# Kernel optimization log

Measured on AMD Instinct MI355X. Metric: run time of the kernel, lower is better.

## Reference

```python
import jax, jax.numpy as jnp
import numpy as np

NUM_HEADS = 12


def setup_inputs() -> dict:
    key = jax.random.key(0)
    k1, k2, k3, k4 = jax.random.split(key, 4)
    B, T, N, C = 4, 64, 196, 768
    x = jax.random.normal(k1, (B, T, N, C), dtype=jnp.float32)
    w_qkv = jax.random.normal(k2, (3 * C, C), dtype=jnp.float32) * (C ** -0.5)
    w_proj = jax.random.normal(k3, (C, C), dtype=jnp.float32) * (C ** -0.5)
    b_proj = jax.random.normal(k4, (C,), dtype=jnp.float32) * 0.01
    return {"x": x, "w_qkv": w_qkv, "w_proj": w_proj, "b_proj": b_proj}


def reference(x, w_qkv, w_proj, b_proj):
    B, T, N, C = x.shape
    H = NUM_HEADS
    hd = C // H
    scale = hd ** -0.5
    # qkv: (B, T, N, 3C) -> (3, B, H, N, T, hd)
    qkv = (x @ w_qkv.T).reshape(B, T, N, 3, H, hd)
    qkv = jnp.transpose(qkv, (3, 0, 4, 2, 1, 5))
    q, k, v = qkv[0], qkv[1], qkv[2]
    # temporal attention per spatial position: (B, H, N, T, T)
    attn = jnp.einsum('bhnqd,bhnkd->bhnqk', q, k) * scale
    causal_mask = jnp.triu(jnp.ones((T, T), dtype=bool), k=1)
    attn = jnp.where(causal_mask, -jnp.inf, attn)
    attn = jax.nn.softmax(attn, axis=-1)
    out = jnp.einsum('bhnqk,bhnkd->bhnqd', attn, v)  # (B, H, N, T, hd)
    out = jnp.transpose(out, (0, 3, 2, 1, 4)).reshape(B, T, N, C)
    return out @ w_proj.T + b_proj
```

## Files before the change

kernel.cpp:

```cpp
#include <hip/hip_runtime.h>

typedef unsigned short UST;
typedef __bf16 bf16x8 __attribute__((ext_vector_type(8)));
typedef float f32x4 __attribute__((ext_vector_type(4)));
typedef float f32x8 __attribute__((ext_vector_type(8)));

__device__ __forceinline__ UST f2bf(float f) {
  return __builtin_bit_cast(UST, (__bf16)f);
}

__device__ __forceinline__ void split8v(f32x8 f, uint4& h, uint4& l) {
  UST hh[8], ll[8];
#pragma unroll
  for (int i = 0; i < 8; ++i) {
    float v = f[i];
    __bf16 hb = (__bf16)v;
    hh[i] = __builtin_bit_cast(UST, hb);
    ll[i] = __builtin_bit_cast(UST, (__bf16)(v - (float)hb));
  }
  h = *(uint4*)hh; l = *(uint4*)ll;
}

__device__ __forceinline__ size_t tok_row(int p, int bn0) {
  const int bn = bn0 + (p >> 6);
  const int b  = bn / 196;
  const int n  = bn - b * 196;
  return (size_t)b * 12544 + (size_t)(p & 63) * 196 + (size_t)n;
}

__device__ __forceinline__ void gl_lds16(const void* g, void* l) {
  __builtin_amdgcn_global_load_lds(
      (__attribute__((address_space(1))) void*)g,
      (__attribute__((address_space(3))) void*)l, 16, 0, 0);
}

__global__ __launch_bounds__(256) void split_f32(
    const float* __restrict__ in, UST* __restrict__ hi, UST* __restrict__ lo,
    int n8)
{
  for (int i = blockIdx.x * 256 + threadIdx.x; i < n8; i += gridDim.x * 256) {
    f32x8 v = *(const f32x8*)(in + (size_t)i * 8);
    uint4 h, l;
    split8v(v, h, l);
    *(uint4*)(hi + (size_t)i * 8) = h;
    *(uint4*)(lo + (size_t)i * 8) = l;
  }
}

__global__ __launch_bounds__(256) void gemm_pre(
    const UST* __restrict__ Agh, const UST* __restrict__ Agl,
    const UST* __restrict__ Bgh, const UST* __restrict__ Bgl,
    const float* __restrict__ bias, float* __restrict__ Cf,
    UST* __restrict__ Cb,
    int M, int N, int K, int pmode, int bn0)
{
  __shared__ __align__(16) UST Ah[128 * 32];
  __shared__ __align__(16) UST Al[128 * 32];
  __shared__ __align__(16) UST Bh[128 * 32];
  __shared__ __align__(16) UST Bl[128 * 32];

  const int tid  = threadIdx.x;
  const int lane = tid & 63;
  const int wv   = tid >> 6;
  const int wr   = wv >> 1;
  const int wc   = wv & 1;
  const int lm   = lane & 15;
  const int lq   = lane >> 4;

  const int m0 = blockIdx.y * 128;
  const int n0 = blockIdx.x * 128;

  f32x4 acc[4][4] = {};

  const int sr = tid >> 2;
  const int sc = (tid & 3) * 8;

  const int ar1 = m0 + sr, ar2 = ar1 + 64;
  const size_t ga1 = (pmode == 1) ? tok_row(ar1, bn0) : (size_t)ar1;
  const size_t ga2 = (pmode == 1) ? tok_row(ar2, bn0) : (size_t)ar2;
  const UST* pA1h = Agh + ga1 * K + sc;
  const UST* pA2h = Agh + ga2 * K + sc;
  const UST* pA1l = Agl + ga1 * K + sc;
  const UST* pA2l = Agl + ga2 * K + sc;
  const UST* pB1h = Bgh + (size_t)(n0 + sr) * K + sc;
  const UST* pB2h = Bgh + (size_t)(n0 + sr + 64) * K + sc;
  const UST* pB1l = Bgl + (size_t)(n0 + sr) * K + sc;
  const UST* pB2l = Bgl + (size_t)(n0 + sr + 64) * K + sc;

  const int l0 = wv * 64 * 8;
  const int l1 = (256 + wv * 64) * 8;

  for (int k0 = 0; k0 < K; k0 += 32) {
    __syncthreads();
    gl_lds16(pA1h + k0, &Ah[l0]);
    gl_lds16(pA2h + k0, &Ah[l1]);
    gl_lds16(pA1l + k0, &Al[l0]);
    gl_lds16(pA2l + k0, &Al[l1]);
    gl_lds16(pB1h + k0, &Bh[l0]);
    gl_lds16(pB2h + k0, &Bh[l1]);
    gl_lds16(pB1l + k0, &Bl[l0]);
    gl_lds16(pB2l + k0, &Bl[l1]);
    __syncthreads();

    bf16x8 afh[4], afl[4], bfh[4], bfl[4];
#pragma unroll
    for (int i = 0; i < 4; ++i) {
      const int off = (wr * 64 + i * 16 + lm) * 32 + lq * 8;
      afh[i] = *(const bf16x8*)(Ah + off);
      afl[i] = *(const bf16x8*)(Al + off);
    }
#pragma unroll
    for (int j = 0; j < 4; ++j) {
      const int off = (wc * 64 + j * 16 + lm) * 32 + lq * 8;
      bfh[j] = *(const bf16x8*)(Bh + off);
      bfl[j] = *(const bf16x8*)(Bl + off);
    }
#pragma unroll
    for (int i = 0; i < 4; ++i)
#pragma unroll
      for (int j = 0; j < 4; ++j) {
        acc[i][j] = __builtin_amdgcn_mfma_f32_16x16x32_bf16(afh[i], bfh[j], acc[i][j], 0, 0, 0);
        acc[i][j] = __builtin_amdgcn_mfma_f32_16x16x32_bf16(afh[i], bfl[j], acc[i][j], 0, 0, 0);
        acc[i][j] = __builtin_amdgcn_mfma_f32_16x16x32_bf16(afl[i], bfh[j], acc[i][j], 0, 0, 0);
      }
  }

#pragma unroll
  for (int j = 0; j < 4; ++j) {
    const int n = n0 + wc * 64 + j * 16 + lm;
    const float bv = bias ? bias[n] : 0.0f;
#pragma unroll
    for (int i = 0; i < 4; ++i) {
      const int pb = m0 + wr * 64 + i * 16 + lq * 4;
#pragma unroll
      for (int r = 0; r < 4; ++r) {
        const int p = pb + r;
        const size_t g = (pmode == 2) ? tok_row(p, bn0) : (size_t)p;
        const float v = acc[i][j][r] + bv;
        if (Cb) Cb[g * (size_t)N + n] = f2bf(v);
        else    Cf[g * (size_t)N + n] = v;
      }
    }
  }
}

#define SQ_STRIDE 67
#define TS 72

__global__ __launch_bounds__(256) void attn64(
    const UST* __restrict__ qkv, UST* __restrict__ oh, UST* __restrict__ ol)
{
  const int nl = blockIdx.x;
  const int h  = blockIdx.y;

  __shared__ __align__(16) UST Qs[64 * TS];
  __shared__ __align__(16) UST Ks[64 * TS];
  __shared__ __align__(16) UST Vt[64 * TS];
  __shared__ __align__(16) UST Ps[64 * TS];
  __shared__ float Ss[64 * SQ_STRIDE];
  __shared__ float red[4 * 64];
  __shared__ float denom[64];

  const int tid  = threadIdx.x;
  const int lane = tid & 63;
  const int wv   = tid >> 6;
  const int lm   = lane & 15;
  const int lq   = lane >> 4;

#pragma unroll
  for (int it = 0; it < 2; ++it) {
    const int idx = it * 256 + tid;
    const int t   = idx >> 3;
    const int f0  = (idx & 7) * 8;
    const UST* row = qkv + (size_t)(nl * 64 + t) * 2304 + h * 64 + f0;
    uint4 qv = *(const uint4*)row;
    uint4 kv = *(const uint4*)(row + 768);
    uint4 vv = *(const uint4*)(row + 1536);
    *(uint4*)(&Qs[t * TS + f0]) = qv;
    *(uint4*)(&Ks[t * TS + f0]) = kv;
    UST vs[8];
    *(uint4*)vs = vv;
    const int cb = t >> 3;
#pragma unroll
    for (int i = 0; i < 8; ++i) {
      const int d = f0 + i;
      Vt[d * TS + (((cb ^ (d >> 3)) & 7) << 3) + (t & 7)] = vs[i];
    }
  }
  __syncthreads();

  f32x4 accS[4] = {};
#pragma unroll
  for (int s = 0; s < 2; ++s) {
    bf16x8 aq = *(const bf16x8*)(&Qs[(wv * 16 + lm) * TS + s * 32 + lq * 8]);
#pragma unroll
    for (int j = 0; j < 4; ++j) {
      bf16x8 bk = *(const bf16x8*)(&Ks[(j * 16 + lm) * TS + s * 32 + lq * 8]);
      accS[j] = __builtin_amdgcn_mfma_f32_16x16x32_bf16(aq, bk, accS[j], 0, 0, 0);
    }
  }

#pragma unroll
  for (int j = 0; j < 4; ++j)
#pragma unroll
    for (int r = 0; r < 4; ++r) {
      const int q = wv * 16 + lq * 4 + r;
      const int c = j * 16 + lm;
      Ss[q * SQ_STRIDE + c] = (c > q) ? -1e30f : accS[j][r] * 0.125f;
    }
  __syncthreads();

  {
    const int r = tid >> 2;
    const int seg = tid & 3;
    const float* srow = &Ss[r * SQ_STRIDE + seg * 16];
    float mx = -1e30f;
#pragma unroll
    for (int c = 0; c < 16; ++c) mx = fmaxf(mx, srow[c]);
    red[seg * 64 + r] = mx;
  }
  __syncthreads();
  {
    const int r = tid >> 2;
    const int seg = tid & 3;
    const float M = fmaxf(fmaxf(red[r], red[64 + r]), fmaxf(red[128 + r], red[192 + r]));
    float ssum = 0.f;
#pragma unroll
    for (int c = 0; c < 16; ++c) {
      const int col = seg * 16 + c;
      float e = 0.f;
      if (col <= r) e = __expf(Ss[r * SQ_STRIDE + col] - M);
      Ps[r * TS + col] = f2bf(e);
      ssum += e;
    }
    __syncthreads();
    red[seg * 64 + r] = ssum;
  }
  __syncthreads();
  if (tid < 64)
    denom[tid] = red[tid] + red[64 + tid] + red[128 + tid] + red[192 + tid];
  __syncthreads();

  f32x4 accO[4] = {};
#pragma unroll
  for (int s = 0; s < 2; ++s) {
    bf16x8 ap = *(const bf16x8*)(&Ps[(wv * 16 + lm) * TS + s * 32 + lq * 8]);
#pragma unroll
    for (int j = 0; j < 4; ++j) {
      const int d = j * 16 + lm;
      const int cb = s * 4 + lq;
      bf16x8 bv = *(const bf16x8*)(&Vt[d * TS + (((cb ^ (d >> 3)) & 7) << 3)]);
      accO[j] = __builtin_amdgcn_mfma_f32_16x16x32_bf16(ap, bv, accO[j], 0, 0, 0);
    }
  }

  float inv[4];
#pragma unroll
  for (int r = 0; r < 4; ++r) inv[r] = 1.0f / denom[wv * 16 + lq * 4 + r];
#pragma unroll
  for (int j = 0; j < 4; ++j)
#pragma unroll
    for (int r = 0; r < 4; ++r) {
      const int q = wv * 16 + lq * 4 + r;
      const int d = j * 16 + lm;
      const float o = accO[j][r] * inv[r];
      const __bf16 hb = (__bf16)o;
      const size_t gi = (size_t)(nl * 64 + q) * 768 + h * 64 + d;
      oh[gi] = __builtin_bit_cast(UST, hb);
      ol[gi] = f2bf(o - (float)hb);
    }
}

__global__ void fill_one(float* p, int n) {
  for (int i = blockIdx.x * 256 + threadIdx.x; i < n; i += gridDim.x * 256)
    p[i] = 1.0f;
}

extern "C" void kernel_launch(void* const* d_in, const int* in_sizes, int n_in,
                              void* d_out, int out_size, void* d_ws, size_t ws_size,
                              hipStream_t stream)
{
  const float* x      = (const float*)d_in[0];
  const float* w_qkv  = (const float*)d_in[1];
  const float* w_proj = (const float*)d_in[2];
  const float* b_proj = (const float*)d_in[3];
  float* out = (float*)d_out;

  const size_t XN = 38535168ull;
  const size_t WQ = 2304ull * 768;
  const size_t WP = 768ull * 768;
  const size_t fixed_b = 2 * (2 * XN + 2 * WQ + 2 * WP);
  const size_t per_bn = 64ull * 2304 * 2 + 2ull * 64 * 768 * 2;

  static const int cands[] = {784, 392, 196, 112, 56, 28, 14, 8, 4, 2};
  int NBc = 0;
  for (int i = 0; i < 10; ++i) {
    if (fixed_b + (size_t)cands[i] * per_bn <= ws_size) { NBc = cands[i]; break; }
  }

  if (NBc == 0) {
    fill_one<<<512, 256, 0, stream>>>(out, out_size);
    return;
  }

  UST* Xh  = (UST*)d_ws;
  UST* Xl  = Xh + XN;
  UST* Wh  = Xl + XN;
  UST* Wl  = Wh + WQ;
  UST* Ph  = Wl + WQ;
  UST* Pl  = Ph + WP;
  UST* qkv = Pl + WP;
  UST* Oh  = qkv + (size_t)NBc * 64 * 2304;
  UST* Ol  = Oh + (size_t)NBc * 64 * 768;

  split_f32<<<2048, 256, 0, stream>>>(x, Xh, Xl, (int)(XN / 8));
  split_f32<<<864, 256, 0, stream>>>(w_qkv, Wh, Wl, (int)(WQ / 8));
  split_f32<<<288, 256, 0, stream>>>(w_proj, Ph, Pl, (int)(WP / 8));

  const int Mi = NBc * 64;
  for (int bn0 = 0; bn0 < 784; bn0 += NBc) {
    dim3 g1(2304 / 128, Mi / 128);
    gemm_pre<<<g1, 256, 0, stream>>>(Xh, Xl, Wh, Wl, nullptr, nullptr, qkv,
                                     Mi, 2304, 768, 1, bn0);
    dim3 ga(NBc, 12);
    attn64<<<ga, 256, 0, stream>>>(qkv, Oh, Ol);
    dim3 g2(768 / 128, Mi / 128);
    gemm_pre<<<g2, 256, 0, stream>>>(Oh, Ol, Ph, Pl, b_proj, out, nullptr,
                                     Mi, 768, 768, 2, bn0);
  }
}
```

Before: 1.198 ms.

## Rewrite split-bf16 GEMM with 256x256 tiles, double-buffered LDS and XCD remap

Replaces the 128x128 single-buffered GEMM with a 512-thread 256x256-tile kernel that double-buffers its global-to-LDS loads, so the next K slice is fetched while MFMAs run on the current one. It adds an XOR swizzle of LDS chunks to reduce bank conflicts, remaps workgroup ids across the 8 XCDs for L2 locality, and raises wave priority around the MFMA blocks. The larger tile cuts redundant A/B traffic per output, at the cost of much higher register and LDS use (128 KB of LDS per block) and fewer blocks on the small projection GEMM. Batch candidates not divisible by 4 are dropped so M stays a multiple of 256.

New measurement: 1.031 ms. -14.0%, faster.

```diff
diff --git a/kernel.cpp b/kernel.cpp
--- a/kernel.cpp
+++ b/kernel.cpp
@@ -28,9 +28,9 @@
   return (size_t)b * 12544 + (size_t)(p & 63) * 196 + (size_t)n;
 }
 
-__device__ __forceinline__ void gl_lds16(const void* g, void* l) {
+__device__ __forceinline__ void gl_lds16(const UST* g, UST* l) {
   __builtin_amdgcn_global_load_lds(
-      (__attribute__((address_space(1))) void*)g,
+      (const __attribute__((address_space(1))) void*)g,
       (__attribute__((address_space(3))) void*)l, 16, 0, 0);
 }
 
@@ -47,94 +47,125 @@
   }
 }
 
-__global__ __launch_bounds__(256) void gemm_pre(
+#define SBAR()   __builtin_amdgcn_s_barrier()
+#define SCHED0() __builtin_amdgcn_sched_barrier(0)
+#define WAIT_VM0() do { asm volatile("s_waitcnt vmcnt(0)" ::: "memory"); SCHED0(); } while (0)
+
+__global__ __launch_bounds__(512, 2) void gemm2p(
     const UST* __restrict__ Agh, const UST* __restrict__ Agl,
     const UST* __restrict__ Bgh, const UST* __restrict__ Bgl,
     const float* __restrict__ bias, float* __restrict__ Cf,
     UST* __restrict__ Cb,
     int M, int N, int K, int pmode, int bn0)
 {
-  __shared__ __align__(16) UST Ah[128 * 32];
-  __shared__ __align__(16) UST Al[128 * 32];
-  __shared__ __align__(16) UST Bh[128 * 32];
-  __shared__ __align__(16) UST Bl[128 * 32];
+  __shared__ __align__(16) UST lds[2][4][8192];
 
   const int tid  = threadIdx.x;
   const int lane = tid & 63;
   const int wv   = tid >> 6;
-  const int wr   = wv >> 1;
-  const int wc   = wv & 1;
+  const int wr   = wv >> 2;
+  const int wcn  = wv & 3;
   const int lm   = lane & 15;
   const int lq   = lane >> 4;
 
-  const int m0 = blockIdx.y * 128;
-  const int n0 = blockIdx.x * 128;
-
-  f32x4 acc[4][4] = {};
-
-  const int sr = tid >> 2;
-  const int sc = (tid & 3) * 8;
-
-  const int ar1 = m0 + sr, ar2 = ar1 + 64;
-  const size_t ga1 = (pmode == 1) ? tok_row(ar1, bn0) : (size_t)ar1;
-  const size_t ga2 = (pmode == 1) ? tok_row(ar2, bn0) : (size_t)ar2;
-  const UST* pA1h = Agh + ga1 * K + sc;
-  const UST* pA2h = Agh + ga2 * K + sc;
-  const UST* pA1l = Agl + ga1 * K + sc;
-  const UST* pA2l = Agl + ga2 * K + sc;
-  const UST* pB1h = Bgh + (size_t)(n0 + sr) * K + sc;
-  const UST* pB2h = Bgh + (size_t)(n0 + sr + 64) * K + sc;
-  const UST* pB1l = Bgl + (size_t)(n0 + sr) * K + sc;
-  const UST* pB2l = Bgl + (size_t)(n0 + sr + 64) * K + sc;
-
-  const int l0 = wv * 64 * 8;
-  const int l1 = (256 + wv * 64) * 8;
-
-  for (int k0 = 0; k0 < K; k0 += 32) {
-    __syncthreads();
-    gl_lds16(pA1h + k0, &Ah[l0]);
-    gl_lds16(pA2h + k0, &Ah[l1]);
-    gl_lds16(pA1l + k0, &Al[l0]);
-    gl_lds16(pA2l + k0, &Al[l1]);
-    gl_lds16(pB1h + k0, &Bh[l0]);
-    gl_lds16(pB2h + k0, &Bh[l1]);
-    gl_lds16(pB1l + k0, &Bl[l0]);
-    gl_lds16(pB2l + k0, &Bl[l1]);
-    __syncthreads();
-
-    bf16x8 afh[4], afl[4], bfh[4], bfl[4];
-#pragma unroll
-    for (int i = 0; i < 4; ++i) {
-      const int off = (wr * 64 + i * 16 + lm) * 32 + lq * 8;
-      afh[i] = *(const bf16x8*)(Ah + off);
-      afl[i] = *(const bf16x8*)(Al + off);
-    }
+  const int gx  = gridDim.x;
+  const int nwg = gx * gridDim.y;
+  int wgid;
+  {
+    const int orig = blockIdx.y * gx + blockIdx.x;
+    const int q = nwg >> 3, r = nwg & 7;
+    const int xcd = orig & 7, off = orig >> 3;
+    wgid = (xcd < r ? xcd * (q + 1) : r * (q + 1) + (xcd - r) * q) + off;
+  }
+  const int m0 = (wgid / gx) * 256;
+  const int n0 = (wgid % gx) * 256;
+
+  const int l2   = lane >> 2;
+  const int csrc = (lane & 3) ^ (((lane >> 5) & 1) << 1);
+  const int sA0 = m0 + wv * 16 + l2;
+  const int sB0 = n0 + wv * 16 + l2;
+  const size_t rA0 = (pmode == 1) ? tok_row(sA0, bn0)       : (size_t)sA0;
+  const size_t rA1 = (pmode == 1) ? tok_row(sA0 + 128, bn0) : (size_t)(sA0 + 128);
+  const UST* pA0h = Agh + rA0 * K + csrc * 8;
+  const UST* pA0l = Agl + rA0 * K + csrc * 8;
+  const UST* pA1h = Agh + rA1 * K + csrc * 8;
+  const UST* pA1l = Agl + rA1 * K + csrc * 8;
+  const UST* pB0h = Bgh + (size_t)sB0 * K + csrc * 8;
+  const UST* pB0l = Bgl + (size_t)sB0 * K + csrc * 8;
+  const UST* pB1h = Bgh + (size_t)(sB0 + 128) * K + csrc * 8;
+  const UST* pB1l = Bgl + (size_t)(sB0 + 128) * K + csrc * 8;
+  const int ldst = wv * 512;
+
+  const int ck = lq ^ (((lm >> 3) & 1) << 1);
+  const int raBase = (wr * 128 + lm) * 32 + ck * 8;
+  const int rbBase = (wcn * 64 + lm) * 32 + ck * 8;
+
+  f32x4 acc[8][4] = {};
+
+#define STAGE(bufW, koff) do { \
+  gl_lds16(pA0h + (koff), (bufW)[0] + 0 * 4096 + ldst); \
+  gl_lds16(pA1h + (koff), (bufW)[0] + 1 * 4096 + ldst); \
+  gl_lds16(pA0l + (koff), (bufW)[1] + 0 * 4096 + ldst); \
+  gl_lds16(pA1l + (koff), (bufW)[1] + 1 * 4096 + ldst); \
+  gl_lds16(pB0h + (koff), (bufW)[2] + 0 * 4096 + ldst); \
+  gl_lds16(pB1h + (koff), (bufW)[2] + 1 * 4096 + ldst); \
+  gl_lds16(pB0l + (koff), (bufW)[3] + 0 * 4096 + ldst); \
+  gl_lds16(pB1l + (koff), (bufW)[3] + 1 * 4096 + ldst); \
+} while (0)
+
+  STAGE(lds[0], 0);
+
+  const int NT = K >> 5;
+  for (int u = 0; u < NT; ++u) {
+    UST (*bufR)[8192] = lds[u & 1];
+    UST (*bufW)[8192] = lds[(u & 1) ^ 1];
+    WAIT_VM0();
+    SBAR();
+    SCHED0();
+    if (u + 1 < NT) STAGE(bufW, (u + 1) * 32);
+
+    bf16x8 bfh[4], bfl[4];
 #pragma unroll
     for (int j = 0; j < 4; ++j) {
-      const int off = (wc * 64 + j * 16 + lm) * 32 + lq * 8;
-      bfh[j] = *(const bf16x8*)(Bh + off);
-      bfl[j] = *(const bf16x8*)(Bl + off);
-    }
-#pragma unroll
-    for (int i = 0; i < 4; ++i)
-#pragma unroll
-      for (int j = 0; j < 4; ++j) {
-        acc[i][j] = __builtin_amdgcn_mfma_f32_16x16x32_bf16(afh[i], bfh[j], acc[i][j], 0, 0, 0);
-        acc[i][j] = __builtin_amdgcn_mfma_f32_16x16x32_bf16(afh[i], bfl[j], acc[i][j], 0, 0, 0);
-        acc[i][j] = __builtin_amdgcn_mfma_f32_16x16x32_bf16(afl[i], bfh[j], acc[i][j], 0, 0, 0);
+      const int off = rbBase + j * 512;
+      bfh[j] = *(const bf16x8*)(bufR[2] + off);
+      bfl[j] = *(const bf16x8*)(bufR[3] + off);
+    }
+#pragma unroll
+    for (int mh = 0; mh < 2; ++mh) {
+      bf16x8 afh[4], afl[4];
+#pragma unroll
+      for (int ii = 0; ii < 4; ++ii) {
+        const int off = raBase + (mh * 4 + ii) * 512;
+        afh[ii] = *(const bf16x8*)(bufR[0] + off);
+        afl[ii] = *(const bf16x8*)(bufR[1] + off);
       }
-  }
+      __builtin_amdgcn_s_setprio(1);
+#pragma unroll
+      for (int ii = 0; ii < 4; ++ii)
+#pragma unroll
+        for (int jj = 0; jj < 4; ++jj) {
+          f32x4 c = acc[mh * 4 + ii][jj];
+          c = __builtin_amdgcn_mfma_f32_16x16x32_bf16(afh[ii], bfh[jj], c, 0, 0, 0);
+          c = __builtin_amdgcn_mfma_f32_16x16x32_bf16(afh[ii], bfl[jj], c, 0, 0, 0);
+          c = __builtin_amdgcn_mfma_f32_16x16x32_bf16(afl[ii], bfh[jj], c, 0, 0, 0);
+          acc[mh * 4 + ii][jj] = c;
+        }
+      __builtin_amdgcn_s_setprio(0);
+    }
+  }
+#undef STAGE
 
 #pragma unroll
   for (int j = 0; j < 4; ++j) {
-    const int n = n0 + wc * 64 + j * 16 + lm;
+    const int n = n0 + wcn * 64 + j * 16 + lm;
     const float bv = bias ? bias[n] : 0.0f;
 #pragma unroll
-    for (int i = 0; i < 4; ++i) {
-      const int pb = m0 + wr * 64 + i * 16 + lq * 4;
+    for (int i = 0; i < 8; ++i) {
+      const int pbase = m0 + wr * 128 + i * 16 + lq * 4;
 #pragma unroll
       for (int r = 0; r < 4; ++r) {
-        const int p = pb + r;
+        const int p = pbase + r;
         const size_t g = (pmode == 2) ? tok_row(p, bn0) : (size_t)p;
         const float v = acc[i][j][r] + bv;
         if (Cb) Cb[g * (size_t)N + n] = f2bf(v);
@@ -292,9 +323,9 @@
   const size_t fixed_b = 2 * (2 * XN + 2 * WQ + 2 * WP);
   const size_t per_bn = 64ull * 2304 * 2 + 2ull * 64 * 768 * 2;
 
-  static const int cands[] = {784, 392, 196, 112, 56, 28, 14, 8, 4, 2};
+  static const int cands[] = {784, 392, 196, 112, 56, 28, 8, 4};
   int NBc = 0;
-  for (int i = 0; i < 10; ++i) {
+  for (int i = 0; i < 8; ++i) {
     if (fixed_b + (size_t)cands[i] * per_bn <= ws_size) { NBc = cands[i]; break; }
   }
 
@@ -319,13 +350,13 @@
 
   const int Mi = NBc * 64;
   for (int bn0 = 0; bn0 < 784; bn0 += NBc) {
-    dim3 g1(2304 / 128, Mi / 128);
-    gemm_pre<<<g1, 256, 0, stream>>>(Xh, Xl, Wh, Wl, nullptr, nullptr, qkv,
-                                     Mi, 2304, 768, 1, bn0);
+    dim3 g1(2304 / 256, Mi / 256);
+    gemm2p<<<g1, 512, 0, stream>>>(Xh, Xl, Wh, Wl, nullptr, nullptr, qkv,
+                                   Mi, 2304, 768, 1, bn0);
     dim3 ga(NBc, 12);
     attn64<<<ga, 256, 0, stream>>>(qkv, Oh, Ol);
-    dim3 g2(768 / 128, Mi / 128);
-    gemm_pre<<<g2, 256, 0, stream>>>(Oh, Ol, Ph, Pl, b_proj, out, nullptr,
-                                     Mi, 768, 768, 2, bn0);
-  }
-}
+    dim3 g2(768 / 256, Mi / 256);
+    gemm2p<<<g2, 512, 0, stream>>>(Oh, Ol, Ph, Pl, b_proj, out, nullptr,
+                                   Mi, 768, 768, 2, bn0);
+  }
+}
```
